# Performance work log

Hardware: AMD Instinct MI355X
Metric: run time of the kernel (lower is better)

The kernel has to match this reference:

```python
import jax, jax.numpy as jnp
import numpy as np

FEAT_DIM = 1024
NUM_HEAD = 8


def setup_inputs() -> dict:
    key = jax.random.key(0)
    ks = jax.random.split(key, 8)
    D = FEAT_DIM
    s = D ** -0.5
    return {
        "motion": jax.random.normal(ks[0], (8, 1024, D), dtype=jnp.float32),
        "scene_feats": jax.random.normal(ks[1], (8, 2048, D), dtype=jnp.float32),
        # nn.Linear weights stored as [in, out] (already transposed for x @ W)
        "Wq": jax.random.normal(ks[2], (D, D), dtype=jnp.float32) * s,
        "bq": jax.random.normal(ks[3], (D,), dtype=jnp.float32) * s,
        "Wkv": jax.random.normal(ks[4], (D, 2 * D), dtype=jnp.float32) * s,
        "bkv": jax.random.normal(ks[5], (2 * D,), dtype=jnp.float32) * s,
        "Wout": jax.random.normal(ks[6], (D, D), dtype=jnp.float32) * s,
        "bout": jax.random.normal(ks[7], (D,), dtype=jnp.float32) * s,
    }


def reference(motion, scene_feats, Wq, bq, Wkv, bkv, Wout, bout):
    bs, L, D = motion.shape
    N = scene_feats.shape[1]
    H = NUM_HEAD
    Dh = D // H

    # q scaled by full feat_dim**-0.5 (as in source, not head_dim)
    q = (motion @ Wq + bq) * (D ** -0.5)
    kv = scene_feats @ Wkv + bkv
    k, v = kv[..., :D], kv[..., D:]

    # Faithful to source: q is viewed as (bs, H, L, Dh) with NO transpose,
    # while k, v use view(bs, N, H, Dh) followed by transpose(1, 2).
    q = q.reshape(bs, H, L, Dh)                      # [bs,H,L,Dh] (layout quirk)
    k = k.reshape(bs, N, H, Dh).transpose(0, 2, 1, 3)  # [bs,H,N,Dh]
    v = v.reshape(bs, N, H, Dh).transpose(0, 2, 1, 3)  # [bs,H,N,Dh]

    att = jnp.einsum("bhld,bhnd->bhln", q, k)        # [bs,H,L,N]
    att = jax.nn.softmax(att, axis=-1)
    out = jnp.einsum("bhln,bhnd->bhld", att, v)      # [bs,H,L,Dh]
    out = out.reshape(bs, L, D)                      # contiguous view, matches torch .view
    return out @ Wout + bout
```

## Files before the change

kernel.cpp:

```cpp
#include <hip/hip_runtime.h>

typedef __attribute__((ext_vector_type(8))) short bf16x8;
typedef __attribute__((ext_vector_type(4))) float f32x4;
typedef __attribute__((ext_vector_type(4))) float f32x4v;
typedef __attribute__((ext_vector_type(4))) int i32x4;

#define MFMA16(a,b,c) __builtin_amdgcn_mfma_f32_16x16x32_bf16((a),(b),(c),0,0,0)

__device__ __forceinline__ short f2bf(float f){
  unsigned u = __builtin_bit_cast(unsigned, f);
  u += 0x7fffu + ((u >> 16) & 1u);
  return (short)(u >> 16);
}

__device__ __forceinline__ void gload16(const void* g, void* l){
  __builtin_amdgcn_global_load_lds((const __attribute__((address_space(1))) unsigned*)g,
                                   (__attribute__((address_space(3))) unsigned*)l,
                                   16, 0, 0);
}

__device__ __forceinline__ int packbf(float a, float b){
  unsigned ua = __builtin_bit_cast(unsigned, a) + 0x7fffu;
  unsigned ub = __builtin_bit_cast(unsigned, b) + 0x7fffu;
  return __builtin_amdgcn_perm(ub, ua, 0x07060302);
}

__global__ __launch_bounds__(256) void k_f2bf_all(const float* __restrict__ motion,
                                                  const float* __restrict__ scene,
                                                  short* __restrict__ mOut,
                                                  short* __restrict__ sOut){
  int blk = blockIdx.x;
  const float* in; short* out; int i;
  if (blk < 4096){ in = motion; out = mOut; i = blk * 256 + threadIdx.x; }
  else           { in = scene;  out = sOut; i = (blk - 4096) * 256 + threadIdx.x; }
  f32x4v a = ((const f32x4v*)in)[i*2];
  f32x4v b = ((const f32x4v*)in)[i*2+1];
  bf16x8 o;
  o[0]=f2bf(a[0]); o[1]=f2bf(a[1]); o[2]=f2bf(a[2]); o[3]=f2bf(a[3]);
  o[4]=f2bf(b[0]); o[5]=f2bf(b[1]); o[6]=f2bf(b[2]); o[7]=f2bf(b[3]);
  ((bf16x8*)out)[i] = o;
}

__global__ __launch_bounds__(256) void k_prep_all(const float* __restrict__ Wq,
                                                  const float* __restrict__ Wkv,
                                                  const float* __restrict__ Wout,
                                                  short* __restrict__ WqT,
                                                  short* __restrict__ WkvT,
                                                  short* __restrict__ WoutT){
  int blk = blockIdx.x;
  const float* W; short* Wt; int N, i;
  if (blk < 512)       { W = Wq;   Wt = WqT;   N = 1024; i = blk * 256 + threadIdx.x; }
  else if (blk < 1536) { W = Wkv;  Wt = WkvT;  N = 2048; i = (blk - 512) * 256 + threadIdx.x; }
  else                 { W = Wout; Wt = WoutT; N = 1024; i = (blk - 1536) * 256 + threadIdx.x; }
  int n  = i % N;
  int k0 = (i / N) << 3;
  bf16x8 o;
#pragma unroll
  for (int j = 0; j < 8; ++j) o[j] = f2bf(W[(size_t)(k0 + j) * N + n]);
  *(bf16x8*)&Wt[(size_t)n * 1024 + k0] = o;
}

template<int MODE>
__global__ __launch_bounds__(256, 4) void k_gemm(
    const short* __restrict__ A, const short* __restrict__ Bt,
    const float* __restrict__ bias, float scale,
    void* __restrict__ out0, void* __restrict__ out1,
    int M, int N, int K)
{
  __shared__ __align__(16) short Alds[3][128 * 32];
  __shared__ __align__(16) short Blds[3][128 * 32];
  const int tid = threadIdx.x;
  const int l = tid & 63, w = tid >> 6;
  const int wr = w >> 1, wc = w & 1;
  const int lr = l & 15, lg = l >> 4;

  const int nx = gridDim.x;
  const int nwg = nx * gridDim.y;
  int flat = blockIdx.y * nx + blockIdx.x;
  int u = (flat & 7) * (nwg >> 3) + (flat >> 3);
  const int m0 = (u / nx) * 128, n0 = (u % nx) * 128;

  const int srow = l >> 2;
  const int scol = 8 * ((l & 3) ^ ((l >> 3) & 3));
  const int acol = 8 * (lg ^ ((lr >> 1) & 3));

  f32x4 acc[4][4];
#pragma unroll
  for (int a = 0; a < 4; ++a)
#pragma unroll
    for (int b = 0; b < 4; ++b) acc[a][b] = (f32x4)(0.0f);

  const int nk = K >> 5;
  auto stage = [&](int kt, int slot){
    int k0 = kt << 5;
#pragma unroll
    for (int i = 0; i < 4; ++i){
      int c = w * 4 + i;
      if (c < 8){
        int m = c * 16 + srow;
        gload16(A + (size_t)(m0 + m) * K + k0 + scol, &Alds[slot][c * 512]);
      } else {
        int n = (c - 8) * 16 + srow;
        gload16(Bt + (size_t)(n0 + n) * K + k0 + scol, &Blds[slot][(c - 8) * 512]);
      }
    }
  };

  stage(0, 0);
  stage(1, 1);
  int rd = 0;
  for (int kt = 0; kt < nk; ++kt){
    asm volatile("s_waitcnt vmcnt(4)" ::: "memory");
    __builtin_amdgcn_s_barrier();
    __builtin_amdgcn_sched_barrier(0);
    int tt = (kt + 2 < nk) ? kt + 2 : nk - 1;
    int tgt = rd + 2; if (tgt >= 3) tgt -= 3;
    stage(tt, tgt);

    bf16x8 af[4], bfv[4];
#pragma unroll
    for (int mi = 0; mi < 4; ++mi){
      int row = wr * 64 + mi * 16 + lr;
      af[mi] = *(const bf16x8*)&Alds[rd][row * 32 + acol];
    }
#pragma unroll
    for (int ni = 0; ni < 4; ++ni){
      int row = wc * 64 + ni * 16 + lr;
      bfv[ni] = *(const bf16x8*)&Blds[rd][row * 32 + acol];
    }
#pragma unroll
    for (int mi = 0; mi < 4; ++mi)
#pragma unroll
      for (int ni = 0; ni < 4; ++ni)
        acc[mi][ni] = MFMA16(af[mi], bfv[ni], acc[mi][ni]);

    if (++rd == 3) rd = 0;
  }
  asm volatile("s_waitcnt vmcnt(0)" ::: "memory");

#pragma unroll
  for (int mi = 0; mi < 4; ++mi)
#pragma unroll
    for (int ni = 0; ni < 4; ++ni){
      int col = n0 + wc * 64 + ni * 16 + lr;
      float bv = bias[col];
#pragma unroll
      for (int r = 0; r < 4; ++r){
        int row = m0 + wr * 64 + mi * 16 + lg * 4 + r;
        float v = acc[mi][ni][r] + bv;
        if (MODE == 0){
          v *= scale;
          int b = row >> 10, lp = row & 1023;
          int h = lp >> 7;
          int lq = ((lp & 127) << 3) | (col >> 7);
          int dh = col & 127;
          ((short*)out0)[(((size_t)(b * 8 + h)) * 1024 + lq) * 128 + dh] = f2bf(v);
        } else {
          ((float*)out0)[(size_t)row * N + col] = v;
        }
      }
    }
}

__global__ __launch_bounds__(512, 1) void k_gemmKV(
    const short* __restrict__ A, const short* __restrict__ Bt,
    const float* __restrict__ bias,
    short* __restrict__ out0, short* __restrict__ out1)
{
  __shared__ __align__(16) short As[4][256 * 32];
  __shared__ __align__(16) short Bs[4][256 * 32];
  const int tid = threadIdx.x;
  const int l = tid & 63, w = tid >> 6;
  const int lr = l & 15, lg = l >> 4;
  const int wm = w >> 2, wn = w & 3;

  int flat = blockIdx.y * 8 + blockIdx.x;
  int u = (flat & 7) * 64 + (flat >> 3);
  const int m0 = (u >> 3) * 256, n0 = (u & 7) * 256;

  const int srow = l >> 2;
  const int scol = 8 * ((l & 3) ^ ((l >> 3) & 3));
  const int acol = 8 * (lg ^ ((lr >> 1) & 3));

  f32x4 acc[8][4];
#pragma unroll
  for (int a = 0; a < 8; ++a)
#pragma unroll
    for (int b = 0; b < 4; ++b) acc[a][b] = (f32x4)(0.0f);

  auto stage = [&](int kt, int slot){
    int k0 = kt << 5;
#pragma unroll
    for (int i = 0; i < 4; ++i){
      int c = w * 4 + i;
      if (c < 16){
        int m = c * 16 + srow;
        gload16(A + (size_t)(m0 + m) * 1024 + k0 + scol, &As[slot][c * 512]);
      } else {
        int n = (c - 16) * 16 + srow;
        gload16(Bt + (size_t)(n0 + n) * 1024 + k0 + scol, &Bs[slot][(c - 16) * 512]);
      }
    }
  };

  stage(0, 0);
  stage(1, 1);
  stage(2, 2);
  int rd = 0;
  for (int kt = 0; kt < 32; ++kt){
    asm volatile("s_waitcnt vmcnt(8)" ::: "memory");
    __builtin_amdgcn_s_barrier();
    __builtin_amdgcn_sched_barrier(0);
    int tt = (kt + 3 < 32) ? kt + 3 : 31;
    stage(tt, (rd + 3) & 3);

    bf16x8 af[8], bfv[4];
#pragma unroll
    for (int mi = 0; mi < 8; ++mi){
      int row = wm * 128 + mi * 16 + lr;
      af[mi] = *(const bf16x8*)&As[rd][row * 32 + acol];
    }
#pragma unroll
    for (int ni = 0; ni < 4; ++ni){
      int row = wn * 64 + ni * 16 + lr;
      bfv[ni] = *(const bf16x8*)&Bs[rd][row * 32 + acol];
    }
    __builtin_amdgcn_s_setprio(1);
#pragma unroll
    for (int mi = 0; mi < 8; ++mi)
#pragma unroll
      for (int ni = 0; ni < 4; ++ni)
        acc[mi][ni] = MFMA16(af[mi], bfv[ni], acc[mi][ni]);
    __builtin_amdgcn_s_setprio(0);

    rd = (rd + 1) & 3;
  }
  asm volatile("s_waitcnt vmcnt(0)" ::: "memory");

#pragma unroll
  for (int mi = 0; mi < 8; ++mi)
#pragma unroll
    for (int ni = 0; ni < 4; ++ni){
      int col = n0 + wn * 64 + ni * 16 + lr;
      float bv = bias[col];
#pragma unroll
      for (int r = 0; r < 4; ++r){
        int row = m0 + wm * 128 + mi * 16 + lg * 4 + r;
        float v = acc[mi][ni][r] + bv;
        int b = row >> 11, nn = row & 2047;
        if (col < 1024){
          int h = col >> 7, dh = col & 127;
          out0[(((size_t)(b * 8 + h)) * 2048 + nn) * 128 + dh] = f2bf(v);
        } else {
          int c2 = col - 1024, h = c2 >> 7, dh = c2 & 127;
          out1[(((size_t)(b * 8 + h)) * 128 + dh) * 2048 + nn] = f2bf(v);
        }
      }
    }
}

__global__ __launch_bounds__(256, 2) void k_attn(
    const short* __restrict__ Q, const short* __restrict__ K,
    const short* __restrict__ Vt, short* __restrict__ O)
{
  __shared__ __align__(16) short Klds[2][64 * 128];
  __shared__ __align__(16) short Vlds[2][128 * 64];
  const int tid = threadIdx.x;
  const int l = tid & 63, w = tid >> 6;
  const int lr = l & 15, lg = l >> 4;

  int flat = blockIdx.y * 8 + blockIdx.x;
  int xcd = flat & 7, idx = flat >> 3;
  int bh = xcd * 8 + (idx >> 3);
  int q0 = (idx & 7) * 128;
  const int qbase = q0 + w * 32;

  const short* Qb = Q  + (size_t)bh * 1024 * 128;
  const short* Kb = K  + (size_t)bh * 2048 * 128;
  const short* Vb = Vt + (size_t)bh * 128 * 2048;

  bf16x8 qf[2][4];
#pragma unroll
  for (int mi = 0; mi < 2; ++mi)
#pragma unroll
    for (int kc = 0; kc < 4; ++kc)
      qf[mi][kc] = *(const bf16x8*)&Qb[(size_t)(qbase + mi * 16 + lr) * 128 + kc * 32 + lg * 8];

  f32x4 acc[2][8];
#pragma unroll
  for (int mi = 0; mi < 2; ++mi)
#pragma unroll
    for (int d = 0; d < 8; ++d) acc[mi][d] = (f32x4)(0.0f);
  float mrun[2] = {-3e38f, -3e38f}, lsum[2] = {0.f, 0.f};

  const int addrA = 4 * ((l & 15) + 32 * ((l >> 4) & 1));
  const int addrB = addrA + 64;
  const bool hi = (l >= 32);

  auto stageK = [&](int t, int buf){
    int kv0 = t * 64;
#pragma unroll
    for (int i = 0; i < 4; ++i){
      int c = w * 4 + i;
      int row = 4 * c + (l >> 4);
      int col = ((l & 15) * 8) ^ ((row & 7) * 8);
      gload16(Kb + (size_t)(kv0 + row) * 128 + col, &Klds[buf][c * 512]);
    }
  };
  auto stageV = [&](int t, int buf){
    int kv0 = t * 64;
#pragma unroll
    for (int i = 0; i < 4; ++i){
      int c = w * 4 + i;
      int dh = 8 * c + (l >> 3);
      int col = ((l & 7) * 8) ^ (((l >> 3) & 7) * 8);
      gload16(Vb + (size_t)dh * 2048 + kv0 + col, &Vlds[buf][c * 512]);
    }
  };

  stageK(0, 0); stageV(0, 0);
  __syncthreads();
  int cur = 0;
  const int swz = (lr & 7) * 8;

  for (int t = 0; t < 32; ++t){
    if (t + 1 < 32){ stageK(t + 1, cur ^ 1); stageV(t + 1, cur ^ 1); }
    const short* Kl = &Klds[cur][0];
    const short* Vl = &Vlds[cur][0];

    f32x4 s[2][4];
    __builtin_amdgcn_s_setprio(1);
#pragma unroll
    for (int nt = 0; nt < 4; ++nt){
      f32x4 s0 = (f32x4)(0.0f), s1 = (f32x4)(0.0f);
#pragma unroll
      for (int kc = 0; kc < 4; ++kc){
        bf16x8 kf = *(const bf16x8*)&Kl[(nt * 16 + lr) * 128 + ((kc * 32 + lg * 8) ^ swz)];
        s0 = MFMA16(kf, qf[0][kc], s0);
        s1 = MFMA16(kf, qf[1][kc], s1);
      }
      s[0][nt] = s0; s[1][nt] = s1;
    }
    __builtin_amdgcn_s_setprio(0);

    float mloc[2];
    int ok = 1;
#pragma unroll
    for (int mi = 0; mi < 2; ++mi){
      float v = fmaxf(fmaxf(fmaxf(s[mi][0][0], s[mi][0][1]), fmaxf(s[mi][0][2], s[mi][0][3])),
                      fmaxf(fmaxf(s[mi][1][0], s[mi][1][1]), fmaxf(s[mi][1][2], s[mi][1][3])));
      v = fmaxf(v, fmaxf(fmaxf(fmaxf(s[mi][2][0], s[mi][2][1]), fmaxf(s[mi][2][2], s[mi][2][3])),
                         fmaxf(fmaxf(s[mi][3][0], s[mi][3][1]), fmaxf(s[mi][3][2], s[mi][3][3]))));
      mloc[mi] = v;
      ok &= (v <= mrun[mi] + 8.0f) ? 1 : 0;
    }
    if (!__all(ok)){
#pragma unroll
      for (int mi = 0; mi < 2; ++mi){
        float v = mloc[mi];
        v = fmaxf(v, __shfl_xor(v, 16));
        v = fmaxf(v, __shfl_xor(v, 32));
        float mnew = fmaxf(mrun[mi], v);
        float sc = exp2f(mrun[mi] - mnew);
        mrun[mi] = mnew;
        lsum[mi] *= sc;
#pragma unroll
        for (int r = 0; r < 4; ++r){
          float scr = __shfl(sc, 20 * lg + r);
#pragma unroll
          for (int d = 0; d < 8; ++d) acc[mi][d][r] *= scr;
        }
      }
    }

    int pk[2][4][2];
#pragma unroll
    for (int mi = 0; mi < 2; ++mi){
      float ls = 0.f;
#pragma unroll
      for (int nt = 0; nt < 4; ++nt){
        float p0 = exp2f(s[mi][nt][0] - mrun[mi]);
        float p1 = exp2f(s[mi][nt][1] - mrun[mi]);
        float p2 = exp2f(s[mi][nt][2] - mrun[mi]);
        float p3 = exp2f(s[mi][nt][3] - mrun[mi]);
        ls += (p0 + p1) + (p2 + p3);
        pk[mi][nt][0] = packbf(p0, p1);
        pk[mi][nt][1] = packbf(p2, p3);
      }
      lsum[mi] += ls;
    }

    bf16x8 pa[2][2];
#pragma unroll
    for (int mi = 0; mi < 2; ++mi)
#pragma unroll
      for (int kc = 0; kc < 2; ++kc){
        i32x4 dw;
#pragma unroll
        for (int av = 0; av < 2; ++av){
          int addr = av ? addrB : addrA;
#pragma unroll
          for (int jj = 0; jj < 2; ++jj){
            int t0 = __builtin_amdgcn_ds_bpermute(addr, pk[mi][2 * kc][jj]);
            int t1 = __builtin_amdgcn_ds_bpermute(addr, pk[mi][2 * kc + 1][jj]);
            dw[av * 2 + jj] = hi ? t1 : t0;
          }
        }
        pa[mi][kc] = __builtin_bit_cast(bf16x8, dw);
      }

    __builtin_amdgcn_s_setprio(1);
#pragma unroll
    for (int d = 0; d < 8; ++d)
#pragma unroll
      for (int kc = 0; kc < 2; ++kc){
        bf16x8 vf = *(const bf16x8*)&Vl[(d * 16 + lr) * 64 + ((kc * 32 + lg * 8) ^ swz)];
        acc[0][d] = MFMA16(pa[0][kc], vf, acc[0][d]);
        acc[1][d] = MFMA16(pa[1][kc], vf, acc[1][d]);
      }
    __builtin_amdgcn_s_setprio(0);

    __syncthreads();
    cur ^= 1;
  }

  const int b = bh >> 3, h = bh & 7;
#pragma unroll
  for (int mi = 0; mi < 2; ++mi){
    float ls = lsum[mi];
    ls += __shfl_xor(ls, 16);
    ls += __shfl_xor(ls, 32);
    float inv = 1.0f / ls;
#pragma unroll
    for (int r = 0; r < 4; ++r){
      float invr = __shfl(inv, 20 * lg + r);
      int grow = qbase + mi * 16 + lg * 4 + r;
      size_t base = ((size_t)b * 1024 + (size_t)h * 128 + (grow >> 3)) * 1024
                  + (size_t)(grow & 7) * 128;
#pragma unroll
      for (int d = 0; d < 8; ++d)
        O[base + d * 16 + lr] = f2bf(acc[mi][d][r] * invr);
    }
  }
}

extern "C" void kernel_launch(void* const* d_in, const int* in_sizes, int n_in,
                              void* d_out, int out_size, void* d_ws, size_t ws_size,
                              hipStream_t stream){
  const float* motion = (const float*)d_in[0];
  const float* scene  = (const float*)d_in[1];
  const float* Wq     = (const float*)d_in[2];
  const float* bq     = (const float*)d_in[3];
  const float* Wkv    = (const float*)d_in[4];
  const float* bkv    = (const float*)d_in[5];
  const float* Wout   = (const float*)d_in[6];
  const float* bout   = (const float*)d_in[7];
  float* out = (float*)d_out;

  char* ws = (char*)d_ws;
  const size_t MB = 1024 * 1024;
  short* WqT   = (short*)(ws + 0);
  short* WkvT  = (short*)(ws + 2  * MB);
  short* WoutT = (short*)(ws + 6  * MB);
  short* mA    = (short*)(ws + 8  * MB);
  short* sA    = (short*)(ws + 24 * MB);
  short* Qb    = (short*)(ws + 56 * MB);
  short* Kb    = (short*)(ws + 72 * MB);
  short* Vtb   = (short*)(ws + 104* MB);
  short* attnO = mA;

  const float qscale = 0.03125f * 1.44269504088896341f;

  k_prep_all<<<dim3(2048), 256, 0, stream>>>(Wq, Wkv, Wout, WqT, WkvT, WoutT);
  k_f2bf_all<<<dim3(12288), 256, 0, stream>>>(motion, scene, mA, sA);

  k_gemm<0><<<dim3(8, 64), 256, 0, stream>>>(mA, WqT, bq, qscale, Qb, nullptr, 8192, 1024, 1024);
  k_gemmKV<<<dim3(8, 64), 512, 0, stream>>>(sA, WkvT, bkv, Kb, Vtb);
  k_attn<<<dim3(8, 64), 256, 0, stream>>>(Qb, Kb, Vtb, attnO);
  k_gemm<2><<<dim3(8, 64), 256, 0, stream>>>(attnO, WoutT, bout, 1.0f, out, nullptr, 8192, 1024, 1024);
}
```

Baseline: 296.5 us.

## Restructure KV projection GEMM into double-buffered K=64 tiles with phased staging

The KV projection GEMM moves from a 4-slot ring of K=32 tiles to 2 slots of K=64 tiles, with an 8-way XOR swizzle in shared memory. Each iteration is split into four phases, one per N sub-tile. The next A and B half-tiles are issued between phases so global-to-LDS loads overlap MFMA work, and barriers bracket each phase. This halves the number of main-loop iterations and per-tile barrier overhead, but adds more barriers per iteration and makes the load/compute interleaving more fragile.

```diff
diff --git a/kernel.cpp b/kernel.cpp
--- a/kernel.cpp
+++ b/kernel.cpp
@@ -167,8 +167,8 @@
     const float* __restrict__ bias,
     short* __restrict__ out0, short* __restrict__ out1)
 {
-  __shared__ __align__(16) short As[4][256 * 32];
-  __shared__ __align__(16) short Bs[4][256 * 32];
+  __shared__ __align__(16) short As[2][256 * 64];
+  __shared__ __align__(16) short Bs[2][256 * 64];
   const int tid = threadIdx.x;
   const int l = tid & 63, w = tid >> 6;
   const int lr = l & 15, lg = l >> 4;
@@ -178,9 +178,25 @@
   int u = (flat & 7) * 64 + (flat >> 3);
   const int m0 = (u >> 3) * 256, n0 = (u & 7) * 256;
 
-  const int srow = l >> 2;
-  const int scol = 8 * ((l & 3) ^ ((l >> 3) & 3));
-  const int acol = 8 * (lg ^ ((lr >> 1) & 3));
+  const int srow = l >> 3;
+  const int scol = (((l & 7) ^ ((l >> 3) & 7)) * 8);
+
+  auto stageA = [&](int tt, int h, int slot){
+#pragma unroll
+    for (int i = 0; i < 2; ++i){
+      int c = w * 2 + i;
+      gload16(A + (size_t)(m0 + h * 128 + c * 8 + srow) * 1024 + tt * 64 + scol,
+              &As[slot][(h * 128 + c * 8) * 64]);
+    }
+  };
+  auto stageB = [&](int tt, int h, int slot){
+#pragma unroll
+    for (int i = 0; i < 2; ++i){
+      int c = w * 2 + i;
+      gload16(Bt + (size_t)(n0 + h * 128 + c * 8 + srow) * 1024 + tt * 64 + scol,
+              &Bs[slot][(h * 128 + c * 8) * 64]);
+    }
+  };
 
   f32x4 acc[8][4];
 #pragma unroll
@@ -188,54 +204,75 @@
 #pragma unroll
     for (int b = 0; b < 4; ++b) acc[a][b] = (f32x4)(0.0f);
 
-  auto stage = [&](int kt, int slot){
-    int k0 = kt << 5;
-#pragma unroll
-    for (int i = 0; i < 4; ++i){
-      int c = w * 4 + i;
-      if (c < 16){
-        int m = c * 16 + srow;
-        gload16(A + (size_t)(m0 + m) * 1024 + k0 + scol, &As[slot][c * 512]);
-      } else {
-        int n = (c - 16) * 16 + srow;
-        gload16(Bt + (size_t)(n0 + n) * 1024 + k0 + scol, &Bs[slot][(c - 16) * 512]);
-      }
-    }
-  };
-
-  stage(0, 0);
-  stage(1, 1);
-  stage(2, 2);
-  int rd = 0;
-  for (int kt = 0; kt < 32; ++kt){
-    asm volatile("s_waitcnt vmcnt(8)" ::: "memory");
-    __builtin_amdgcn_s_barrier();
-    __builtin_amdgcn_sched_barrier(0);
-    int tt = (kt + 3 < 32) ? kt + 3 : 31;
-    stage(tt, (rd + 3) & 3);
-
-    bf16x8 af[8], bfv[4];
+#define KV_PHASE(p, B0, B1)                                            \
+  __builtin_amdgcn_s_barrier(); __builtin_amdgcn_sched_barrier(0);     \
+  __builtin_amdgcn_s_setprio(1);                                       \
+  _Pragma("unroll")                                                    \
+  for (int mi = 0; mi < 8; ++mi){                                      \
+    acc[mi][p] = MFMA16(af[mi][0], B0, acc[mi][p]);                    \
+    acc[mi][p] = MFMA16(af[mi][1], B1, acc[mi][p]);                    \
+  }                                                                    \
+  __builtin_amdgcn_s_setprio(0);                                       \
+  __builtin_amdgcn_s_barrier(); __builtin_amdgcn_sched_barrier(0);
+
+  stageA(0, 0, 0); stageA(0, 1, 0);
+  stageB(0, 0, 0); stageB(0, 1, 0);
+  stageA(1, 0, 1); stageA(1, 1, 1);
+  asm volatile("s_waitcnt vmcnt(4)" ::: "memory");
+  __builtin_amdgcn_s_barrier();
+  __builtin_amdgcn_sched_barrier(0);
+
+  for (int t = 0; t < 16; ++t){
+    const int s = t & 1;
+    const short* Asl = &As[s][0];
+    const short* Bsl = &Bs[s][0];
+    const int t1 = (t + 1 < 16) ? t + 1 : 15;
+    const int t2 = (t + 2 < 16) ? t + 2 : 15;
+
+    bf16x8 af[8][2];
 #pragma unroll
     for (int mi = 0; mi < 8; ++mi){
       int row = wm * 128 + mi * 16 + lr;
-      af[mi] = *(const bf16x8*)&As[rd][row * 32 + acol];
-    }
-#pragma unroll
-    for (int ni = 0; ni < 4; ++ni){
-      int row = wn * 64 + ni * 16 + lr;
-      bfv[ni] = *(const bf16x8*)&Bs[rd][row * 32 + acol];
-    }
-    __builtin_amdgcn_s_setprio(1);
-#pragma unroll
-    for (int mi = 0; mi < 8; ++mi)
-#pragma unroll
-      for (int ni = 0; ni < 4; ++ni)
-        acc[mi][ni] = MFMA16(af[mi], bfv[ni], acc[mi][ni]);
-    __builtin_amdgcn_s_setprio(0);
-
-    rd = (rd + 1) & 3;
+#pragma unroll
+      for (int kk = 0; kk < 2; ++kk)
+        af[mi][kk] = *(const bf16x8*)&Asl[row * 64 + (((kk * 4 + lg) ^ (lr & 7)) * 8)];
+    }
+    bf16x8 b0, b1;
+    {
+      int row = wn * 64 + 0 * 16 + lr;
+      b0 = *(const bf16x8*)&Bsl[row * 64 + (((0 + lg) ^ (lr & 7)) * 8)];
+      b1 = *(const bf16x8*)&Bsl[row * 64 + (((4 + lg) ^ (lr & 7)) * 8)];
+    }
+    stageB(t1, 0, s ^ 1);
+    KV_PHASE(0, b0, b1)
+
+    {
+      int row = wn * 64 + 1 * 16 + lr;
+      b0 = *(const bf16x8*)&Bsl[row * 64 + (((0 + lg) ^ (lr & 7)) * 8)];
+      b1 = *(const bf16x8*)&Bsl[row * 64 + (((4 + lg) ^ (lr & 7)) * 8)];
+    }
+    stageB(t1, 1, s ^ 1);
+    KV_PHASE(1, b0, b1)
+
+    {
+      int row = wn * 64 + 2 * 16 + lr;
+      b0 = *(const bf16x8*)&Bsl[row * 64 + (((0 + lg) ^ (lr & 7)) * 8)];
+      b1 = *(const bf16x8*)&Bsl[row * 64 + (((4 + lg) ^ (lr & 7)) * 8)];
+    }
+    stageA(t2, 0, s);
+    KV_PHASE(2, b0, b1)
+
+    {
+      int row = wn * 64 + 3 * 16 + lr;
+      b0 = *(const bf16x8*)&Bsl[row * 64 + (((0 + lg) ^ (lr & 7)) * 8)];
+      b1 = *(const bf16x8*)&Bsl[row * 64 + (((4 + lg) ^ (lr & 7)) * 8)];
+    }
+    stageA(t2, 1, s);
+    asm volatile("s_waitcnt vmcnt(4)" ::: "memory");
+    KV_PHASE(3, b0, b1)
   }
   asm volatile("s_waitcnt vmcnt(0)" ::: "memory");
+#undef KV_PHASE
 
 #pragma unroll
   for (int mi = 0; mi < 8; ++mi)
```

Result: slower. 306.2 us (+3.3%).
